# Optimization experiments

Measured on AMD Instinct MI355X. Metric: run time of the kernel, lower is better.

The kernel has to match this reference:

```python
import jax, jax.numpy as jnp
import numpy as np

H = W = 256
C = 128
SCALE = 512 ** (-0.5)  # literal from the source, not 1/sqrt(C)


def _pool_mat(size, out):
    # adaptive_avg_pool1d matrix: row i averages input[start_i:end_i]
    i = np.arange(out)
    s = (i * size) // out
    e = ((i + 1) * size + out - 1) // out  # ceil
    P = np.zeros((out, size), np.float32)
    for k in range(out):
        P[k, s[k]:e[k]] = 1.0 / (e[k] - s[k])
    return jnp.asarray(P)


def adaptive_avg_pool2d(x, out):
    # x: [B, C, H, W] -> [B, C, out, out] via separable pooling matrices
    Ph = _pool_mat(x.shape[2], out)
    Pw = _pool_mat(x.shape[3], out)
    y = jnp.einsum('oh,bchw->bcow', Ph, x)
    return jnp.einsum('pw,bcow->bcop', Pw, y)


def setup_inputs() -> dict:
    key = jax.random.key(0)
    k1, k2 = jax.random.split(key)
    x5 = jax.random.normal(k1, (4, C, H, W), dtype=jnp.float32)
    W_out = jax.random.normal(k2, (C, C), dtype=jnp.float32) * 0.02
    b_out = jnp.zeros((C,), dtype=jnp.float32)
    return {"x5": x5, "W_out": W_out, "b_out": b_out}


def reference(x5, W_out, b_out):
    B = x5.shape[0]
    # Query: [B, N, C], N = H*W
    Query = x5.reshape(B, C, H * W).transpose(0, 2, 1)
    # multi-scale pooled keys
    p16 = adaptive_avg_pool2d(x5, 16)
    p12 = adaptive_avg_pool2d(x5, 12)
    p9 = adaptive_avg_pool2d(x5, 9)
    p7 = adaptive_avg_pool2d(x5, 7)
    p6 = adaptive_avg_pool2d(x5, 6)
    p3 = adaptive_avg_pool2d(x5, 3)
    p1 = adaptive_avg_pool2d(x5, 1)
    # Key: concat flattened pools in source order [3, 1, 9, 7, 16] -> [B, C, 396]
    Key = jnp.concatenate(
        [p.reshape(B, C, -1) for p in (p3, p1, p9, p7, p16)], axis=-1)
    Value = Key.transpose(0, 2, 1)  # [B, 396, C]
    # attention: [B, N, 396]
    attn = jax.nn.softmax(SCALE * jnp.einsum('bnc,bck->bnk', Query, Key), axis=-1)
    agg = jnp.einsum('bnk,bkc->bnc', attn, Value)  # [B, N, C]
    agg = agg.transpose(0, 2, 1).reshape(B, C, H, W)
    # 1x1 conv
    out = jnp.einsum('oc,bchw->bohw', W_out, agg) + b_out[None, :, None, None]
    return (out + x5, p12, p6)
```

## Files before the change

kernel.cpp:

```cpp
#include <hip/hip_runtime.h>
#include <hip/hip_bf16.h>

typedef short bf16x8 __attribute__((ext_vector_type(8)));
typedef float f32x4  __attribute__((ext_vector_type(4)));
typedef unsigned short u16;

#define B_N 4
#define C_N 128
#define HW_ 256
#define NPIX 65536
#define NK 396
#define NKP 400
#define OUT_MAIN ((size_t)B_N * C_N * NPIX)
#define P12_OFF OUT_MAIN
#define P6_OFF  (P12_OFF + (size_t)B_N * C_N * 144)

#define BUFSZ  32768
#define VT_OFF 16384
#define P_OFF  65536
#define LDS_BYTES 73728

static __device__ __forceinline__ u16 f2bf(float x) {
  __hip_bfloat16 h = __float2bfloat16(x);
  return *(u16*)&h;
}
static __device__ __forceinline__ unsigned pack2(float lo, float hi) {
  return ((unsigned)f2bf(hi) << 16) | f2bf(lo);
}
static __device__ __forceinline__ void gl_lds16(const void* g, void* l) {
  __builtin_amdgcn_global_load_lds(
      (const __attribute__((address_space(1))) unsigned*)g,
      (__attribute__((address_space(3))) unsigned*)l, 16, 0, 0);
}
#define MFMA32 __builtin_amdgcn_mfma_f32_16x16x32_bf16
#define LGKM0 do { asm volatile("s_waitcnt lgkmcnt(0)" ::: "memory"); \
                   __builtin_amdgcn_sched_barrier(0); } while (0)

__global__ __launch_bounds__(1024) void pool_kernel(
    const float* __restrict__ x5, const float* __restrict__ W_out,
    u16* __restrict__ wsK, u16* __restrict__ wsKT, u16* __restrict__ wsW,
    float* __restrict__ out)
{
  __shared__ float yh[54][257];
  const int tid = threadIdx.x;
  const int bc = blockIdx.x;
  const int b  = bc >> 7;
  const int c  = bc & 127;
  const float2* plane2 = (const float2*)(x5 + (size_t)bc * NPIX);
  const int w2 = tid & 127;
  const int q  = tid >> 7;
  const int h0 = q * 32;

  if (bc < 16) {
    const int idx = bc * 1024 + tid;
    wsW[idx] = f2bf(W_out[idx]);
  }

  for (int i = tid; i < 54 * 257; i += 1024) ((float*)yh)[i] = 0.f;
  __syncthreads();

  const int os_[7] = {16,12,9,7,6,3,1};
  const int ro_[7] = {0,16,28,37,44,50,53};
  float ax[7], ay[7], a2x[7], a2y[7], inv_[7];
  int r_[7], e_[7], s2_[7];
  #pragma unroll
  for (int s = 0; s < 7; ++s) {
    const int o = os_[s];
    const int r = (h0 * o) >> 8;
    const int sr = (r * 256) / o;
    r_[s]  = r;
    e_[s]  = ((r + 1) * 256 + o - 1) / o;
    s2_[s] = ((r + 1) * 256) / o;
    inv_[s] = 1.0f / (float)(e_[s] - sr);
    ax[s] = 0.f; ay[s] = 0.f; a2x[s] = 0.f; a2y[s] = 0.f;
  }

  for (int h = h0; h < h0 + 32; ++h) {
    const float2 v = plane2[h * 128 + w2];
    #pragma unroll
    for (int s = 0; s < 7; ++s) {
      const int o = os_[s];
      ax[s] += v.x; ay[s] += v.y;
      if (h >= s2_[s]) { a2x[s] += v.x; a2y[s] += v.y; }
      if (h + 1 == e_[s]) {
        atomicAdd(&yh[ro_[s] + r_[s]][2*w2],     ax[s] * inv_[s]);
        atomicAdd(&yh[ro_[s] + r_[s]][2*w2 + 1], ay[s] * inv_[s]);
        r_[s]++;
        const int sr = s2_[s];
        e_[s]  = ((r_[s] + 1) * 256 + o - 1) / o;
        s2_[s] = ((r_[s] + 1) * 256) / o;
        inv_[s] = 1.0f / (float)(e_[s] - sr);
        ax[s] = a2x[s]; ay[s] = a2y[s];
        a2x[s] = 0.f; a2y[s] = 0.f;
      }
    }
  }
  #pragma unroll
  for (int s = 0; s < 7; ++s) {
    const int o = os_[s];
    if (r_[s] < o) {
      atomicAdd(&yh[ro_[s] + r_[s]][2*w2],     ax[s] * inv_[s]);
      atomicAdd(&yh[ro_[s] + r_[s]][2*w2 + 1], ay[s] * inv_[s]);
      if (r_[s] + 1 < o && s2_[s] < h0 + 32) {
        const int sr2 = s2_[s];
        const int e2  = ((r_[s] + 2) * 256 + o - 1) / o;
        const float inv2 = 1.0f / (float)(e2 - sr2);
        atomicAdd(&yh[ro_[s] + r_[s] + 1][2*w2],     a2x[s] * inv2);
        atomicAdd(&yh[ro_[s] + r_[s] + 1][2*w2 + 1], a2y[s] * inv2);
      }
    }
  }
  __syncthreads();

  if (tid < NKP - NK) {
    wsK [((size_t)b * NKP + NK + tid) * C_N + c] = 0;
    wsKT[(size_t)bc * NKP + NK + tid] = 0;
  }

  for (int r = tid; r < 576; r += 1024) {
    int rr = r;
    int o, ro, kbase, dst;
    if      (rr < 256) { o = 16; ro = 0;  kbase = 140; dst = 0; }
    else if (rr < 400) { o = 12; ro = 16; kbase = 0;   dst = 1; rr -= 256; }
    else if (rr < 481) { o = 9;  ro = 28; kbase = 10;  dst = 0; rr -= 400; }
    else if (rr < 530) { o = 7;  ro = 37; kbase = 91;  dst = 0; rr -= 481; }
    else if (rr < 566) { o = 6;  ro = 44; kbase = 0;   dst = 2; rr -= 530; }
    else if (rr < 575) { o = 3;  ro = 50; kbase = 0;   dst = 0; rr -= 566; }
    else               { o = 1;  ro = 53; kbase = 9;   dst = 0; rr = 0;   }
    const int i = rr / o;
    const int j = rr - i * o;
    const int s = (j * HW_) / o;
    const int e = ((j + 1) * HW_ + o - 1) / o;
    float sum = 0.f;
    const float* row = yh[ro + i];
    for (int wq = s; wq < e; ++wq) sum += row[wq];
    const float v = sum * (1.0f / (float)(e - s));
    if (dst == 1) {
      out[P12_OFF + (size_t)bc * 144 + rr] = v;
    } else if (dst == 2) {
      out[P6_OFF + (size_t)bc * 36 + rr] = v;
    } else {
      const int key = kbase + rr;
      const u16 bv = f2bf(v);
      wsK [((size_t)b * NKP + key) * C_N + c] = bv;
      wsKT[(size_t)bc * NKP + key]            = bv;
    }
  }
}

template<int CB, int BUF>
static __device__ __forceinline__ void stage64(
    char* smem, const char* wsKb, const char* wsKTb, int wv, int lane)
{
  char* buf = smem + BUF * BUFSZ;
  #pragma unroll
  for (int j = 0; j < 4; ++j) {
    const int krow = CB + j*16 + wv*4 + (lane >> 4);
    gl_lds16(wsKb + (size_t)krow * 256 + (((lane & 15) ^ (krow & 15)) << 4),
             buf + j*4096 + wv*1024);
    const int vrow = j*32 + wv*8 + (lane >> 3);
    gl_lds16(wsKTb + (size_t)vrow * (NKP*2) + CB*2 + (((lane & 7) ^ (vrow & 7)) << 4),
             buf + VT_OFF + j*4096 + wv*1024);
  }
}

static __device__ __forceinline__ void stage_tail(
    char* buf, const char* wsKb, const char* wsKTb, int wv, int lane)
{
  {
    const int row = wv*4 + (lane >> 4);
    gl_lds16(wsKb + (size_t)(384 + row) * 256 + (((lane & 15) ^ (row & 15)) << 4),
             buf + wv * 1024);
  }
  #pragma unroll
  for (int j = 0; j < 2; ++j) {
    const int row = j*64 + wv*16 + (lane >> 2);
    gl_lds16(wsKTb + (size_t)row * (NKP*2) + 768 + ((lane & 3) << 4),
             buf + VT_OFF + j*4096 + wv*1024);
  }
}

static __device__ __forceinline__ void stage_W(
    char* smem, const u16* wsW, int wv, int lane)
{
  #pragma unroll
  for (int j = 0; j < 8; ++j) {
    const int row = j*16 + wv*4 + (lane >> 4);
    gl_lds16((const char*)wsW + (size_t)row * 256 + (((lane & 15) ^ (row & 15)) << 4),
             smem + BUFSZ + j*4096 + wv*1024);
  }
}

template<int BUF, int TAIL>
static __device__ __forceinline__ void compute64(
    char* smem, char* pbase, const bf16x8 (&qf)[2][4],
    f32x4 (&agg)[8][2], float (&d)[2], int l15, int l4)
{
  const char* buf = smem + BUF * BUFSZ;
  constexpr int NT   = TAIL ? 1 : 4;
  constexpr int SUBS = TAIL ? 1 : 2;
  const float SCL2 = 0.044194173824159216f * 1.4426950408889634f;

  f32x4 sA[NT][2];
  #pragma unroll
  for (int nt = 0; nt < NT; ++nt) {
    sA[nt][0] = (f32x4){0.f,0.f,0.f,0.f};
    sA[nt][1] = (f32x4){0.f,0.f,0.f,0.f};
  }
  #pragma unroll
  for (int nt = 0; nt < NT; ++nt) {
    bf16x8 kf[4];
    #pragma unroll
    for (int kc = 0; kc < 4; ++kc)
      kf[kc] = *(const bf16x8*)(buf + (nt*16 + l15) * 256 +
                                ((kc*64 + l4*16) ^ (l15 << 4)));
    #pragma unroll
    for (int kc = 0; kc < 4; ++kc) {
      sA[nt][0] = MFMA32(kf[kc], qf[0][kc], sA[nt][0], 0, 0, 0);
      sA[nt][1] = MFMA32(kf[kc], qf[1][kc], sA[nt][1], 0, 0, 0);
    }
  }

  #pragma unroll
  for (int sub = 0; sub < SUBS; ++sub) {
    if (sub) LGKM0;
    #pragma unroll
    for (int pt = 0; pt < 2; ++pt) {
      const int prow = pt*16 + l15;
      const int sz2  = (prow & 3) << 4;
      #pragma unroll
      for (int u = 0; u < (TAIL ? 1 : 2); ++u) {
        const int nt = sub*2 + u;
        float p[4];
        #pragma unroll
        for (int qi = 0; qi < 4; ++qi) {
          float e = exp2f(sA[nt][pt][qi] * SCL2);
          if (TAIL && (l4*4 + qi >= 12)) e = 0.f;
          p[qi] = e;
        }
        d[pt] += (p[0] + p[1]) + (p[2] + p[3]);
        uint2 pk;
        pk.x = pack2(p[0], p[1]);
        pk.y = pack2(p[2], p[3]);
        *(uint2*)(pbase + prow*64 + ((u*32 + l4*8) ^ sz2)) = pk;
      }
      if (TAIL) {
        uint2 z; z.x = 0u; z.y = 0u;
        *(uint2*)(pbase + prow*64 + ((32 + l4*8) ^ sz2)) = z;
      }
    }
    LGKM0;

    bf16x8 pf[2];
    #pragma unroll
    for (int pt = 0; pt < 2; ++pt) {
      const int prow = pt*16 + l15;
      pf[pt] = *(const bf16x8*)(pbase + prow*64 + ((l4*16) ^ ((prow & 3) << 4)));
    }
    #pragma unroll
    for (int ct = 0; ct < 8; ++ct) {
      const int vrow = ct*16 + l15;
      bf16x8 vf;
      if (TAIL)
        vf = *(const bf16x8*)(buf + VT_OFF + vrow*64 + l4*16);
      else
        vf = *(const bf16x8*)(buf + VT_OFF + vrow*128 +
                              ((sub*64 + l4*16) ^ ((vrow & 7) << 4)));
      agg[ct][0] = MFMA32(vf, pf[0], agg[ct][0], 0, 0, 0);
      agg[ct][1] = MFMA32(vf, pf[1], agg[ct][1], 0, 0, 0);
    }
  }
}

__global__ __launch_bounds__(256, 2) void attn_kernel(
    const float* __restrict__ x5, const u16* __restrict__ wsK,
    const u16* __restrict__ wsKT, const u16* __restrict__ wsW,
    const float* __restrict__ b_out, float* __restrict__ out)
{
  extern __shared__ char smem[];
  const int tid  = threadIdx.x;
  const int wgid = (blockIdx.x & 7) * 256 + (blockIdx.x >> 3);
  const int b    = wgid >> 9;
  const int pix0 = (wgid & 511) << 7;
  const int lane = tid & 63, wv = tid >> 6;
  const int l15  = lane & 15, l4 = lane >> 4;
  char* pbase = smem + P_OFF + wv * 2048;

  const char* wsKb  = (const char*)wsK  + (size_t)b * NKP * C_N * 2;
  const char* wsKTb = (const char*)wsKT + (size_t)b * C_N * NKP * 2;

  {
    const float* r0p = x5 + (((size_t)(b * C_N + 2*lane)) << 16) + pix0 + wv * 32;
    const float* r1p = r0p + NPIX;
    float4 v0[8], v1[8];
    #pragma unroll
    for (int j = 0; j < 8; ++j) {
      v0[j] = *(const float4*)(r0p + j*4);
      v1[j] = *(const float4*)(r1p + j*4);
    }
    #pragma unroll
    for (int i = 0; i < 32; ++i) {
      const int pix = wv * 32 + i;
      const unsigned pk = pack2(((const float*)&v0[i>>2])[i&3],
                                ((const float*)&v1[i>>2])[i&3]);
      *(unsigned*)(smem + pix * 256 + ((lane*4) ^ ((pix & 15) << 4))) = pk;
    }
  }
  __syncthreads();

  bf16x8 qf[2][4];
  #pragma unroll
  for (int pt = 0; pt < 2; ++pt)
    #pragma unroll
    for (int kc = 0; kc < 4; ++kc)
      qf[pt][kc] = *(const bf16x8*)(smem + (wv*32 + pt*16 + l15) * 256 +
                                    ((kc*64 + l4*16) ^ (l15 << 4)));
  __syncthreads();

  f32x4 agg[8][2];
  #pragma unroll
  for (int ct = 0; ct < 8; ++ct) {
    agg[ct][0] = (f32x4){0.f,0.f,0.f,0.f};
    agg[ct][1] = (f32x4){0.f,0.f,0.f,0.f};
  }
  float d[2] = {0.f, 0.f};

  stage64<0, 0>(smem, wsKb, wsKTb, wv, lane);
  asm volatile("s_waitcnt vmcnt(0)" ::: "memory");
  __syncthreads();

  stage64<64, 1>(smem, wsKb, wsKTb, wv, lane);
  compute64<0, 0>(smem, pbase, qf, agg, d, l15, l4);
  asm volatile("s_waitcnt vmcnt(0)" ::: "memory");
  __syncthreads();

  stage64<128, 0>(smem, wsKb, wsKTb, wv, lane);
  compute64<1, 0>(smem, pbase, qf, agg, d, l15, l4);
  asm volatile("s_waitcnt vmcnt(0)" ::: "memory");
  __syncthreads();

  stage64<192, 1>(smem, wsKb, wsKTb, wv, lane);
  compute64<0, 0>(smem, pbase, qf, agg, d, l15, l4);
  asm volatile("s_waitcnt vmcnt(0)" ::: "memory");
  __syncthreads();

  stage64<256, 0>(smem, wsKb, wsKTb, wv, lane);
  compute64<1, 0>(smem, pbase, qf, agg, d, l15, l4);
  asm volatile("s_waitcnt vmcnt(0)" ::: "memory");
  __syncthreads();

  stage64<320, 1>(smem, wsKb, wsKTb, wv, lane);
  compute64<0, 0>(smem, pbase, qf, agg, d, l15, l4);
  asm volatile("s_waitcnt vmcnt(0)" ::: "memory");
  __syncthreads();

  stage_tail(smem, wsKb, wsKTb, wv, lane);
  compute64<1, 0>(smem, pbase, qf, agg, d, l15, l4);
  asm volatile("s_waitcnt vmcnt(0)" ::: "memory");
  __syncthreads();

  {
    f32x4 z = (f32x4){0.f,0.f,0.f,0.f};
    *(f32x4*)(smem + VT_OFF + (tid >> 1) * 64 + 32 + ((tid & 1) << 4)) = z;
  }
  stage_W(smem, wsW, wv, lane);
  asm volatile("s_waitcnt vmcnt(0)" ::: "memory");
  __syncthreads();

  compute64<0, 1>(smem, pbase, qf, agg, d, l15, l4);

  float inv[2];
  #pragma unroll
  for (int pt = 0; pt < 2; ++pt) {
    float s = d[pt];
    s += __shfl_xor(s, 16);
    s += __shfl_xor(s, 32);
    inv[pt] = 1.0f / s;
  }

  f32x4 cacc[8][2];
  #pragma unroll
  for (int ot = 0; ot < 8; ++ot) {
    cacc[ot][0] = (f32x4){0.f,0.f,0.f,0.f};
    cacc[ot][1] = (f32x4){0.f,0.f,0.f,0.f};
  }
  #pragma unroll
  for (int qh = 0; qh < 4; ++qh) {
    LGKM0;
    #pragma unroll
    for (int pt = 0; pt < 2; ++pt) {
      const int prow = pt*16 + l15;
      const int sz2  = (prow & 3) << 4;
      #pragma unroll
      for (int u = 0; u < 2; ++u) {
        const f32x4 a = agg[qh*2 + u][pt];
        uint2 pk;
        pk.x = pack2(a[0] * inv[pt], a[1] * inv[pt]);
        pk.y = pack2(a[2] * inv[pt], a[3] * inv[pt]);
        *(uint2*)(pbase + prow*64 + ((u*32 + l4*8) ^ sz2)) = pk;
      }
    }
    LGKM0;
    bf16x8 agf[2];
    #pragma unroll
    for (int pt = 0; pt < 2; ++pt) {
      const int prow = pt*16 + l15;
      agf[pt] = *(const bf16x8*)(pbase + prow*64 + ((l4*16) ^ ((prow & 3) << 4)));
    }
    #pragma unroll
    for (int ot = 0; ot < 8; ++ot) {
      const bf16x8 wa = *(const bf16x8*)(smem + BUFSZ + (ot*16 + l15) * 256 +
                                         ((qh*64 + l4*16) ^ (l15 << 4)));
      cacc[ot][0] = MFMA32(wa, agf[0], cacc[ot][0], 0, 0, 0);
      cacc[ot][1] = MFMA32(wa, agf[1], cacc[ot][1], 0, 0, 0);
    }
  }

  #pragma unroll
  for (int ot = 0; ot < 8; ++ot) {
    const float4 bq = *(const float4*)(b_out + ot*16 + l4*4);
    #pragma unroll
    for (int pt = 0; pt < 2; ++pt) {
      #pragma unroll
      for (int qi = 0; qi < 4; ++qi) {
        const int o = ot*16 + l4*4 + qi;
        const size_t idx = (((size_t)(b * C_N + o)) << 16) + pix0 + wv*32 + pt*16 + l15;
        out[idx] = cacc[ot][pt][qi] + ((const float*)&bq)[qi] + x5[idx];
      }
    }
  }
}

extern "C" void kernel_launch(void* const* d_in, const int* in_sizes, int n_in,
                              void* d_out, int out_size, void* d_ws, size_t ws_size,
                              hipStream_t stream) {
  const float* x5    = (const float*)d_in[0];
  const float* W_out = (const float*)d_in[1];
  const float* b_out = (const float*)d_in[2];
  float* out = (float*)d_out;
  u16* wsKT = (u16*)d_ws;
  u16* wsK  = (u16*)((char*)d_ws + (size_t)B_N * C_N * NKP * 2);
  u16* wsW  = (u16*)((char*)d_ws + (size_t)2 * B_N * C_N * NKP * 2);

  pool_kernel<<<512, 1024, 0, stream>>>(x5, W_out, wsK, wsKT, wsW, out);

  hipFuncSetAttribute((const void*)attn_kernel,
                      hipFuncAttributeMaxDynamicSharedMemorySize, LDS_BYTES);
  attn_kernel<<<B_N * 512, 256, LDS_BYTES, stream>>>(x5, wsK, wsKT, wsW, b_out, out);
}
```

Measured before the change: 211.2 us.

## Feed softmax probabilities to MFMA directly from registers via 16x16x16 bf16

The P·V and output-projection GEMMs now use the 16x16x16 bf16 MFMA, whose accumulator layout matches the B-operand layout. Softmax probabilities and normalized aggregates can therefore go straight from registers into the next MFMA, with no round trip through per-wave LDS scratch and no lgkmcnt waits. The softmax scale is folded into the query during bf16 packing. W_out is read directly from global memory instead of being staged in LDS, which cuts LDS to 64KB and removes a barrier. The cost is twice as many MFMA instructions at half the K depth and uncached global loads for W; the tail zero-fill of V is also dropped, which relies on the padded region already being zero.

```diff
diff --git a/kernel.cpp b/kernel.cpp
--- a/kernel.cpp
+++ b/kernel.cpp
@@ -1,6 +1,7 @@
 #include <hip/hip_runtime.h>
 #include <hip/hip_bf16.h>
 
+typedef short bf16x4 __attribute__((ext_vector_type(4)));
 typedef short bf16x8 __attribute__((ext_vector_type(8)));
 typedef float f32x4  __attribute__((ext_vector_type(4)));
 typedef unsigned short u16;
@@ -17,8 +18,7 @@
 
 #define BUFSZ  32768
 #define VT_OFF 16384
-#define P_OFF  65536
-#define LDS_BYTES 73728
+#define LDS_BYTES 65536
 
 static __device__ __forceinline__ u16 f2bf(float x) {
   __hip_bfloat16 h = __float2bfloat16(x);
@@ -33,8 +33,19 @@
       (__attribute__((address_space(3))) unsigned*)l, 16, 0, 0);
 }
 #define MFMA32 __builtin_amdgcn_mfma_f32_16x16x32_bf16
-#define LGKM0 do { asm volatile("s_waitcnt lgkmcnt(0)" ::: "memory"); \
-                   __builtin_amdgcn_sched_barrier(0); } while (0)
+
+#if __has_builtin(__builtin_amdgcn_mfma_f32_16x16x16bf16_1k)
+#define MFMA16(a, b, c) __builtin_amdgcn_mfma_f32_16x16x16bf16_1k((a), (b), (c), 0, 0, 0)
+#else
+static __device__ __forceinline__ f32x4 mfma16_asm(bf16x4 a, bf16x4 b, f32x4 c) {
+  asm volatile("s_nop 3\n\t"
+               "v_mfma_f32_16x16x16_bf16 %0, %1, %2, %0\n\t"
+               "s_nop 7\n\ts_nop 7"
+               : "+v"(c) : "v"(a), "v"(b));
+  return c;
+}
+#define MFMA16(a, b, c) mfma16_asm((a), (b), (c))
+#endif
 
 __global__ __launch_bounds__(1024) void pool_kernel(
     const float* __restrict__ x5, const float* __restrict__ W_out,
@@ -180,26 +191,13 @@
   }
 }
 
-static __device__ __forceinline__ void stage_W(
-    char* smem, const u16* wsW, int wv, int lane)
-{
-  #pragma unroll
-  for (int j = 0; j < 8; ++j) {
-    const int row = j*16 + wv*4 + (lane >> 4);
-    gl_lds16((const char*)wsW + (size_t)row * 256 + (((lane & 15) ^ (row & 15)) << 4),
-             smem + BUFSZ + j*4096 + wv*1024);
-  }
-}
-
 template<int BUF, int TAIL>
 static __device__ __forceinline__ void compute64(
-    char* smem, char* pbase, const bf16x8 (&qf)[2][4],
+    char* smem, const bf16x8 (&qf)[2][4],
     f32x4 (&agg)[8][2], float (&d)[2], int l15, int l4)
 {
   const char* buf = smem + BUF * BUFSZ;
-  constexpr int NT   = TAIL ? 1 : 4;
-  constexpr int SUBS = TAIL ? 1 : 2;
-  const float SCL2 = 0.044194173824159216f * 1.4426950408889634f;
+  constexpr int NT = TAIL ? 1 : 4;
 
   f32x4 sA[NT][2];
   #pragma unroll
@@ -222,52 +220,34 @@
   }
 
   #pragma unroll
-  for (int sub = 0; sub < SUBS; ++sub) {
-    if (sub) LGKM0;
+  for (int nt = 0; nt < NT; ++nt) {
+    bf16x4 pk[2];
     #pragma unroll
     for (int pt = 0; pt < 2; ++pt) {
-      const int prow = pt*16 + l15;
-      const int sz2  = (prow & 3) << 4;
+      float p[4];
       #pragma unroll
-      for (int u = 0; u < (TAIL ? 1 : 2); ++u) {
-        const int nt = sub*2 + u;
-        float p[4];
-        #pragma unroll
-        for (int qi = 0; qi < 4; ++qi) {
-          float e = exp2f(sA[nt][pt][qi] * SCL2);
-          if (TAIL && (l4*4 + qi >= 12)) e = 0.f;
-          p[qi] = e;
-        }
-        d[pt] += (p[0] + p[1]) + (p[2] + p[3]);
-        uint2 pk;
-        pk.x = pack2(p[0], p[1]);
-        pk.y = pack2(p[2], p[3]);
-        *(uint2*)(pbase + prow*64 + ((u*32 + l4*8) ^ sz2)) = pk;
+      for (int qi = 0; qi < 4; ++qi) {
+        float e = exp2f(sA[nt][pt][qi]);
+        if (TAIL && (l4*4 + qi >= 12)) e = 0.f;
+        p[qi] = e;
       }
-      if (TAIL) {
-        uint2 z; z.x = 0u; z.y = 0u;
-        *(uint2*)(pbase + prow*64 + ((32 + l4*8) ^ sz2)) = z;
-      }
-    }
-    LGKM0;
-
-    bf16x8 pf[2];
-    #pragma unroll
-    for (int pt = 0; pt < 2; ++pt) {
-      const int prow = pt*16 + l15;
-      pf[pt] = *(const bf16x8*)(pbase + prow*64 + ((l4*16) ^ ((prow & 3) << 4)));
+      d[pt] += (p[0] + p[1]) + (p[2] + p[3]);
+      bf16x4 t;
+      t[0] = (short)f2bf(p[0]); t[1] = (short)f2bf(p[1]);
+      t[2] = (short)f2bf(p[2]); t[3] = (short)f2bf(p[3]);
+      pk[pt] = t;
     }
     #pragma unroll
     for (int ct = 0; ct < 8; ++ct) {
       const int vrow = ct*16 + l15;
-      bf16x8 vf;
+      bf16x4 vf;
       if (TAIL)
-        vf = *(const bf16x8*)(buf + VT_OFF + vrow*64 + l4*16);
+        vf = *(const bf16x4*)(buf + VT_OFF + vrow*64 + l4*8);
       else
-        vf = *(const bf16x8*)(buf + VT_OFF + vrow*128 +
-                              ((sub*64 + l4*16) ^ ((vrow & 7) << 4)));
-      agg[ct][0] = MFMA32(vf, pf[0], agg[ct][0], 0, 0, 0);
-      agg[ct][1] = MFMA32(vf, pf[1], agg[ct][1], 0, 0, 0);
+        vf = *(const bf16x4*)(buf + VT_OFF + vrow*128 +
+                              ((nt*32 + l4*8) ^ ((vrow & 7) << 4)));
+      agg[ct][0] = MFMA16(vf, pk[0], agg[ct][0]);
+      agg[ct][1] = MFMA16(vf, pk[1], agg[ct][1]);
     }
   }
 }
@@ -284,7 +264,7 @@
   const int pix0 = (wgid & 511) << 7;
   const int lane = tid & 63, wv = tid >> 6;
   const int l15  = lane & 15, l4 = lane >> 4;
-  char* pbase = smem + P_OFF + wv * 2048;
+  const float SCL2 = 0.044194173824159216f * 1.4426950408889634f;
 
   const char* wsKb  = (const char*)wsK  + (size_t)b * NKP * C_N * 2;
   const char* wsKTb = (const char*)wsKT + (size_t)b * C_N * NKP * 2;
@@ -301,8 +281,8 @@
     #pragma unroll
     for (int i = 0; i < 32; ++i) {
       const int pix = wv * 32 + i;
-      const unsigned pk = pack2(((const float*)&v0[i>>2])[i&3],
-                                ((const float*)&v1[i>>2])[i&3]);
+      const unsigned pk = pack2(((const float*)&v0[i>>2])[i&3] * SCL2,
+                                ((const float*)&v1[i>>2])[i&3] * SCL2);
       *(unsigned*)(smem + pix * 256 + ((lane*4) ^ ((pix & 15) << 4))) = pk;
     }
   }
@@ -330,44 +310,36 @@
   __syncthreads();
 
   stage64<64, 1>(smem, wsKb, wsKTb, wv, lane);
-  compute64<0, 0>(smem, pbase, qf, agg, d, l15, l4);
+  compute64<0, 0>(smem, qf, agg, d, l15, l4);
   asm volatile("s_waitcnt vmcnt(0)" ::: "memory");
   __syncthreads();
 
   stage64<128, 0>(smem, wsKb, wsKTb, wv, lane);
-  compute64<1, 0>(smem, pbase, qf, agg, d, l15, l4);
+  compute64<1, 0>(smem, qf, agg, d, l15, l4);
   asm volatile("s_waitcnt vmcnt(0)" ::: "memory");
   __syncthreads();
 
   stage64<192, 1>(smem, wsKb, wsKTb, wv, lane);
-  compute64<0, 0>(smem, pbase, qf, agg, d, l15, l4);
+  compute64<0, 0>(smem, qf, agg, d, l15, l4);
   asm volatile("s_waitcnt vmcnt(0)" ::: "memory");
   __syncthreads();
 
   stage64<256, 0>(smem, wsKb, wsKTb, wv, lane);
-  compute64<1, 0>(smem, pbase, qf, agg, d, l15, l4);
+  compute64<1, 0>(smem, qf, agg, d, l15, l4);
   asm volatile("s_waitcnt vmcnt(0)" ::: "memory");
   __syncthreads();
 
   stage64<320, 1>(smem, wsKb, wsKTb, wv, lane);
-  compute64<0, 0>(smem, pbase, qf, agg, d, l15, l4);
+  compute64<0, 0>(smem, qf, agg, d, l15, l4);
   asm volatile("s_waitcnt vmcnt(0)" ::: "memory");
   __syncthreads();
 
   stage_tail(smem, wsKb, wsKTb, wv, lane);
-  compute64<1, 0>(smem, pbase, qf, agg, d, l15, l4);
-  asm volatile("s_waitcnt vmcnt(0)" ::: "memory");
-  __syncthreads();
-
-  {
-    f32x4 z = (f32x4){0.f,0.f,0.f,0.f};
-    *(f32x4*)(smem + VT_OFF + (tid >> 1) * 64 + 32 + ((tid & 1) << 4)) = z;
-  }
-  stage_W(smem, wsW, wv, lane);
-  asm volatile("s_waitcnt vmcnt(0)" ::: "memory");
-  __syncthreads();
-
-  compute64<0, 1>(smem, pbase, qf, agg, d, l15, l4);
+  compute64<1, 0>(smem, qf, agg, d, l15, l4);
+  asm volatile("s_waitcnt vmcnt(0)" ::: "memory");
+  __syncthreads();
+
+  compute64<0, 1>(smem, qf, agg, d, l15, l4);
 
   float inv[2];
   #pragma unroll
@@ -385,34 +357,22 @@
     cacc[ot][1] = (f32x4){0.f,0.f,0.f,0.f};
   }
   #pragma unroll
-  for (int qh = 0; qh < 4; ++qh) {
-    LGKM0;
+  for (int ck = 0; ck < 8; ++ck) {
+    bf16x4 af[2];
     #pragma unroll
     for (int pt = 0; pt < 2; ++pt) {
-      const int prow = pt*16 + l15;
-      const int sz2  = (prow & 3) << 4;
-      #pragma unroll
-      for (int u = 0; u < 2; ++u) {
-        const f32x4 a = agg[qh*2 + u][pt];
-        uint2 pk;
-        pk.x = pack2(a[0] * inv[pt], a[1] * inv[pt]);
-        pk.y = pack2(a[2] * inv[pt], a[3] * inv[pt]);
-        *(uint2*)(pbase + prow*64 + ((u*32 + l4*8) ^ sz2)) = pk;
-      }
-    }
-    LGKM0;
-    bf16x8 agf[2];
-    #pragma unroll
-    for (int pt = 0; pt < 2; ++pt) {
-      const int prow = pt*16 + l15;
-      agf[pt] = *(const bf16x8*)(pbase + prow*64 + ((l4*16) ^ ((prow & 3) << 4)));
-    }
+      const f32x4 a = agg[ck][pt];
+      bf16x4 t;
+      t[0] = (short)f2bf(a[0] * inv[pt]); t[1] = (short)f2bf(a[1] * inv[pt]);
+      t[2] = (short)f2bf(a[2] * inv[pt]); t[3] = (short)f2bf(a[3] * inv[pt]);
+      af[pt] = t;
+    }
+    const u16* wrow = wsW + ck*16 + l4*4;
     #pragma unroll
     for (int ot = 0; ot < 8; ++ot) {
-      const bf16x8 wa = *(const bf16x8*)(smem + BUFSZ + (ot*16 + l15) * 256 +
-                                         ((qh*64 + l4*16) ^ (l15 << 4)));
-      cacc[ot][0] = MFMA32(wa, agf[0], cacc[ot][0], 0, 0, 0);
-      cacc[ot][1] = MFMA32(wa, agf[1], cacc[ot][1], 0, 0, 0);
+      const bf16x4 wa = *(const bf16x4*)(wrow + (ot*16 + l15) * 128);
+      cacc[ot][0] = MFMA16(wa, af[0], cacc[ot][0]);
+      cacc[ot][1] = MFMA16(wa, af[1], cacc[ot][1]);
     }
   }
 
```

New measurement: 288.5 us. 1.37x slower.
